# Kernel optimization log

Hardware: AMD Instinct MI355X
Metric: run time of the kernel (lower is better)

The kernel has to match this reference:

```python
import jax, jax.numpy as jnp
import numpy as np

B, C, N, K = 4, 192, 8192, 16
C_OUT = 192


def _gather_nodes(xs, idx):
    # xs: [B, C, N], idx: [B, N, K] -> [B, C, N, K]
    return jax.vmap(lambda xb, ib: xb[:, ib])(xs, idx)


def setup_inputs() -> dict:
    key = jax.random.key(0)
    k1, k2, k3 = jax.random.split(key, 3)
    x = jax.random.normal(k1, (B, C, N, 1), dtype=jnp.float32)
    x_0 = jnp.zeros((B, C, N, 1), dtype=jnp.float32)  # unused by forward, kept for interface
    edge_index = jax.random.randint(k2, (2, B, N, K), 0, N, dtype=jnp.int32)
    # 1x1 Conv2d(2C -> C_OUT) weight flattened to [C_OUT, 2C]
    W = jax.random.normal(k3, (C_OUT, 2 * C), dtype=jnp.float32) / np.sqrt(2 * C)
    b = jnp.zeros((C_OUT,), dtype=jnp.float32)
    return {"x": x, "x_0": x_0, "edge_index": edge_index, "W": W, "b": b}


def reference(x, x_0, edge_index, W, b):
    xs = x[..., 0]                       # [B, C, N]
    x_i = _gather_nodes(xs, edge_index[1])   # centers  [B, C, N, K]
    x_j = _gather_nodes(xs, edge_index[0])   # neighbors [B, C, N, K]
    rel = jnp.max(x_j - x_i, axis=-1)        # max-relative [B, C, N]
    y = jnp.concatenate([xs, rel], axis=1)   # [B, 2C, N]
    out = jnp.einsum('oc,bcn->bon', W, y) + b[None, :, None]  # 1x1 conv
    out = jax.nn.relu(out)
    return out[..., None]                # [B, C_OUT, N, 1]
```

## Files before the change

### kernel.cpp

```cpp
#include <hip/hip_runtime.h>
#include <hip/hip_bf16.h>

#define B_    4
#define C_    192
#define N_    8192
#define K_    16
#define O_    192
#define TWOC_ 384

typedef __attribute__((ext_vector_type(8))) short short8;
typedef __attribute__((ext_vector_type(4))) float floatx4;

static __device__ __forceinline__ float bf2f(unsigned short u) {
    union { unsigned int i; float f; } v; v.i = ((unsigned int)u) << 16; return v.f;
}
static __device__ __forceinline__ unsigned short f2bf(float f) {
    union { float f; unsigned int i; } v; v.f = f;
    unsigned int x = v.i;
    return (unsigned short)((x + 0x7FFFu + ((x >> 16) & 1u)) >> 16);
}

__global__ __launch_bounds__(256) void k_convert_w(const float* __restrict__ W,
                                                   unsigned short* __restrict__ Wb) {
    int i = blockIdx.x * 256 + threadIdx.x;
    if (i < O_ * TWOC_) Wb[i] = f2bf(W[i]);
}

__global__ __launch_bounds__(256) void k_transpose(const float* __restrict__ x,
                                                   unsigned short* __restrict__ yb) {
    __shared__ float tile[32][33];
    int b  = blockIdx.z;
    int c0 = blockIdx.y * 32;
    int n0 = blockIdx.x * 32;
    int tx = threadIdx.x, ty = threadIdx.y;
    const float* xp = x + ((size_t)b * C_ + c0) * N_ + n0;
#pragma unroll
    for (int i = 0; i < 4; i++) {
        int r = ty + 8 * i;
        tile[r][tx] = xp[(size_t)r * N_ + tx];
    }
    __syncthreads();
    unsigned short* yp = yb + ((size_t)b * N_ + n0) * TWOC_ + c0;
#pragma unroll
    for (int i = 0; i < 4; i++) {
        int r = ty + 8 * i;
        yp[(size_t)r * TWOC_ + tx] = f2bf(tile[tx][r]);
    }
}

__global__ __launch_bounds__(256) void k_maxrel(unsigned short* __restrict__ yb,
                                                const int* __restrict__ eidx) {
    int b    = blockIdx.y;
    int wave = threadIdx.x >> 6;
    int lane = threadIdx.x & 63;
    int n    = blockIdx.x * 4 + wave;

    __shared__ int sidx[4][32];
    if (lane < 32) {
        const int* e = eidx + ((size_t)b * N_ + n) * K_;
        int v;
        if (lane < 16) v = e[lane];
        else           v = e[(size_t)B_ * N_ * K_ + (lane - 16)];
        sidx[wave][lane] = v;
    }
    __syncthreads();

    const unsigned short* base = yb + (size_t)b * N_ * TWOC_;
    float m0 = -INFINITY, m1 = -INFINITY, m2 = -INFINITY;
#pragma unroll
    for (int k = 0; k < K_; k++) {
        int j = sidx[wave][k];
        int i = sidx[wave][16 + k];
        const unsigned short* pj = base + (size_t)j * TWOC_;
        const unsigned short* pi = base + (size_t)i * TWOC_;
        float d0 = bf2f(pj[lane])        - bf2f(pi[lane]);
        float d1 = bf2f(pj[lane + 64])   - bf2f(pi[lane + 64]);
        float d2 = bf2f(pj[lane + 128])  - bf2f(pi[lane + 128]);
        m0 = fmaxf(m0, d0);
        m1 = fmaxf(m1, d1);
        m2 = fmaxf(m2, d2);
    }
    unsigned short* w = yb + ((size_t)b * N_ + n) * TWOC_ + C_;
    w[lane]       = f2bf(m0);
    w[lane + 64]  = f2bf(m1);
    w[lane + 128] = f2bf(m2);
}

__global__ __launch_bounds__(64) void k_gemm(const unsigned short* __restrict__ Wb,
                                             const unsigned short* __restrict__ yb,
                                             const float* __restrict__ bias,
                                             float* __restrict__ out) {
    int b    = blockIdx.z;
    int ob   = blockIdx.y;
    int nb   = blockIdx.x;
    int lane = threadIdx.x;
    int m16  = lane & 15;
    int quad = lane >> 4;

    const unsigned short* wbase = Wb + (size_t)(ob * 64 + m16) * TWOC_ + quad * 8;
    const unsigned short* ybase = yb + ((size_t)b * N_ + nb * 64 + m16) * TWOC_ + quad * 8;

    floatx4 acc[4][4];
#pragma unroll
    for (int i = 0; i < 4; i++)
#pragma unroll
        for (int j = 0; j < 4; j++) acc[i][j] = (floatx4){0.f, 0.f, 0.f, 0.f};

#pragma unroll 2
    for (int kt = 0; kt < 12; kt++) {
        short8 af[4], bfr[4];
#pragma unroll
        for (int t = 0; t < 4; t++)
            af[t] = *(const short8*)(wbase + (size_t)(t * 16) * TWOC_ + kt * 32);
#pragma unroll
        for (int t = 0; t < 4; t++)
            bfr[t] = *(const short8*)(ybase + (size_t)(t * 16) * TWOC_ + kt * 32);
#pragma unroll
        for (int i = 0; i < 4; i++)
#pragma unroll
            for (int j = 0; j < 4; j++)
                acc[i][j] = __builtin_amdgcn_mfma_f32_16x16x32_bf16(af[i], bfr[j], acc[i][j], 0, 0, 0);
    }

#pragma unroll
    for (int i = 0; i < 4; i++) {
#pragma unroll
        for (int r = 0; r < 4; r++) {
            int o = ob * 64 + i * 16 + quad * 4 + r;
            float bv = bias[o];
#pragma unroll
            for (int j = 0; j < 4; j++) {
                int n = nb * 64 + j * 16 + m16;
                float v = acc[i][j][r] + bv;
                out[((size_t)b * O_ + o) * N_ + n] = fmaxf(v, 0.f);
            }
        }
    }
}

extern "C" void kernel_launch(void* const* d_in, const int* in_sizes, int n_in,
                              void* d_out, int out_size, void* d_ws, size_t ws_size,
                              hipStream_t stream) {
    const float* x    = (const float*)d_in[0];
    const int*   eidx = (const int*)d_in[2];
    const float* W    = (const float*)d_in[3];
    const float* bias = (const float*)d_in[4];
    float*       out  = (float*)d_out;

    unsigned short* Wb = (unsigned short*)d_ws;
    unsigned short* yb = (unsigned short*)((char*)d_ws + 147456);

    k_convert_w<<<dim3((O_ * TWOC_ + 255) / 256), dim3(256), 0, stream>>>(W, Wb);
    k_transpose<<<dim3(N_ / 32, C_ / 32, B_), dim3(32, 8), 0, stream>>>(x, yb);
    k_maxrel<<<dim3(N_ / 4, B_), dim3(256), 0, stream>>>(yb, eidx);
    k_gemm<<<dim3(N_ / 64, O_ / 64, B_), dim3(64), 0, stream>>>(Wb, yb, bias, out);
}
```

Before: 146.5 us.

## Fuse max-relative gather with GEMM in shared memory, XCD-aware block mapping

Merges the max-relative gather kernel and the 1x1-conv GEMM into one kernel. Each block builds a 64-node tile of [x; rel] in LDS and runs MFMA on it, so the rel half never makes a round trip through global memory. The transpose now writes a compact [B,N,C] bf16 array using vectorized loads and packed stores. Both kernels map blocks so each batch's data stays on a pair of XCDs for L2 locality. The gather loads 4 channels per lane per neighbor. The cost is fewer blocks (512) with a large LDS footprint, which may reduce occupancy and latency hiding for the random gathers.

After: 136.0 us. -7.1%, faster.

```diff
diff --git a/kernel.cpp b/kernel.cpp
--- a/kernel.cpp
+++ b/kernel.cpp
@@ -1,5 +1,4 @@
 #include <hip/hip_runtime.h>
-#include <hip/hip_bf16.h>
 
 #define B_    4
 #define C_    192
@@ -9,10 +8,12 @@
 #define TWOC_ 384
 
 typedef __attribute__((ext_vector_type(8))) short short8;
+typedef __attribute__((ext_vector_type(4))) short short4v;
+typedef __attribute__((ext_vector_type(2))) unsigned int uint2v;
 typedef __attribute__((ext_vector_type(4))) float floatx4;
 
-static __device__ __forceinline__ float bf2f(unsigned short u) {
-    union { unsigned int i; float f; } v; v.i = ((unsigned int)u) << 16; return v.f;
+static __device__ __forceinline__ float bf2f(unsigned int u16) {
+    union { unsigned int i; float f; } v; v.i = u16 << 16; return v.f;
 }
 static __device__ __forceinline__ unsigned short f2bf(float f) {
     union { float f; unsigned int i; } v; v.f = f;
@@ -27,112 +28,155 @@
 }
 
 __global__ __launch_bounds__(256) void k_transpose(const float* __restrict__ x,
-                                                   unsigned short* __restrict__ yb) {
+                                                   unsigned short* __restrict__ xt) {
     __shared__ float tile[32][33];
-    int b  = blockIdx.z;
-    int c0 = blockIdx.y * 32;
-    int n0 = blockIdx.x * 32;
-    int tx = threadIdx.x, ty = threadIdx.y;
-    const float* xp = x + ((size_t)b * C_ + c0) * N_ + n0;
+    int bid  = blockIdx.x;
+    int xcd  = bid & 7;
+    int b    = xcd >> 1;
+    int half = xcd & 1;
+    int slot = bid >> 3;
+    int ct   = slot >> 7;
+    int nt   = half * 128 + (slot & 127);
+    int c0 = ct * 32, n0 = nt * 32;
+    int tid = threadIdx.x;
+
+    int cc  = tid >> 3;
+    int nn4 = (tid & 7) * 4;
+    const float* xp = x + ((size_t)b * C_ + c0 + cc) * N_ + n0 + nn4;
+    float4 v = *(const float4*)xp;
+    tile[nn4 + 0][cc] = v.x;
+    tile[nn4 + 1][cc] = v.y;
+    tile[nn4 + 2][cc] = v.z;
+    tile[nn4 + 3][cc] = v.w;
+    __syncthreads();
+
+#pragma unroll
+    for (int i = 0; i < 2; i++) {
+        int id  = i * 256 + tid;
+        int row = id >> 4;
+        int ch2 = id & 15;
+        float a = tile[row][ch2 * 2];
+        float c = tile[row][ch2 * 2 + 1];
+        unsigned int pack = (unsigned int)f2bf(a) | ((unsigned int)f2bf(c) << 16);
+        *(unsigned int*)(xt + ((size_t)b * N_ + n0 + row) * C_ + c0 + ch2 * 2) = pack;
+    }
+}
+
+__global__ __launch_bounds__(256) void k_fused(const unsigned short* __restrict__ xt,
+                                               const int* __restrict__ eidx,
+                                               const unsigned short* __restrict__ Wb,
+                                               const float* __restrict__ bias,
+                                               float* __restrict__ out) {
+    __shared__ unsigned short ytile[64][TWOC_];
+    __shared__ int sidx[64][33];
+
+    int bid  = blockIdx.x;
+    int xcd  = bid & 7;
+    int b    = xcd >> 1;
+    int slot = bid >> 3;
+    int n0   = ((xcd & 1) * 64 + slot) * 64;
+
+    int tid  = threadIdx.x;
+    int wave = tid >> 6;
+    int lane = tid & 63;
+
+    const int* e0 = eidx + ((size_t)b * N_ + n0) * K_;
+    const int* e1 = e0 + (size_t)B_ * N_ * K_;
 #pragma unroll
     for (int i = 0; i < 4; i++) {
-        int r = ty + 8 * i;
-        tile[r][tx] = xp[(size_t)r * N_ + tx];
+        int id   = i * 256 + tid;
+        int node = id >> 4, k = id & 15;
+        sidx[node][k]      = e0[id];
+        sidx[node][16 + k] = e1[id];
+    }
+
+    const unsigned short* xrow = xt + ((size_t)b * N_ + n0) * C_;
+#pragma unroll
+    for (int i = 0; i < 6; i++) {
+        int id = i * 256 + tid;
+        int row = id / 24, chunk = id % 24;
+        short8 v = *(const short8*)(xrow + (size_t)row * C_ + chunk * 8);
+        *(short8*)&ytile[row][chunk * 8] = v;
     }
     __syncthreads();
-    unsigned short* yp = yb + ((size_t)b * N_ + n0) * TWOC_ + c0;
-#pragma unroll
-    for (int i = 0; i < 4; i++) {
-        int r = ty + 8 * i;
-        yp[(size_t)r * TWOC_ + tx] = f2bf(tile[tx][r]);
-    }
-}
-
-__global__ __launch_bounds__(256) void k_maxrel(unsigned short* __restrict__ yb,
-                                                const int* __restrict__ eidx) {
-    int b    = blockIdx.y;
-    int wave = threadIdx.x >> 6;
-    int lane = threadIdx.x & 63;
-    int n    = blockIdx.x * 4 + wave;
-
-    __shared__ int sidx[4][32];
-    if (lane < 32) {
-        const int* e = eidx + ((size_t)b * N_ + n) * K_;
-        int v;
-        if (lane < 16) v = e[lane];
-        else           v = e[(size_t)B_ * N_ * K_ + (lane - 16)];
-        sidx[wave][lane] = v;
+
+    {
+        int g  = lane >> 4;
+        int l4 = lane & 15;
+        const unsigned short* xbase = xt + (size_t)b * N_ * C_;
+#pragma unroll
+        for (int bb = 0; bb < 4; bb++) {
+            int node = wave * 16 + bb * 4 + g;
+            float m[3][4];
+#pragma unroll
+            for (int t = 0; t < 3; t++)
+#pragma unroll
+                for (int c = 0; c < 4; c++) m[t][c] = -INFINITY;
+#pragma unroll
+            for (int k = 0; k < K_; k++) {
+                int jn = sidx[node][k];
+                int in = sidx[node][16 + k];
+                const unsigned short* pj = xbase + (size_t)jn * C_ + l4 * 4;
+                const unsigned short* pi = xbase + (size_t)in * C_ + l4 * 4;
+#pragma unroll
+                for (int t = 0; t < 3; t++) {
+                    uint2v vj = *(const uint2v*)(pj + t * 64);
+                    uint2v vi = *(const uint2v*)(pi + t * 64);
+                    m[t][0] = fmaxf(m[t][0], bf2f(vj.x & 0xffffu) - bf2f(vi.x & 0xffffu));
+                    m[t][1] = fmaxf(m[t][1], bf2f(vj.x >> 16)     - bf2f(vi.x >> 16));
+                    m[t][2] = fmaxf(m[t][2], bf2f(vj.y & 0xffffu) - bf2f(vi.y & 0xffffu));
+                    m[t][3] = fmaxf(m[t][3], bf2f(vj.y >> 16)     - bf2f(vi.y >> 16));
+                }
+            }
+#pragma unroll
+            for (int t = 0; t < 3; t++) {
+                short4v s;
+                s.x = (short)f2bf(m[t][0]);
+                s.y = (short)f2bf(m[t][1]);
+                s.z = (short)f2bf(m[t][2]);
+                s.w = (short)f2bf(m[t][3]);
+                *(short4v*)&ytile[node][C_ + t * 64 + l4 * 4] = s;
+            }
+        }
     }
     __syncthreads();
 
-    const unsigned short* base = yb + (size_t)b * N_ * TWOC_;
-    float m0 = -INFINITY, m1 = -INFINITY, m2 = -INFINITY;
-#pragma unroll
-    for (int k = 0; k < K_; k++) {
-        int j = sidx[wave][k];
-        int i = sidx[wave][16 + k];
-        const unsigned short* pj = base + (size_t)j * TWOC_;
-        const unsigned short* pi = base + (size_t)i * TWOC_;
-        float d0 = bf2f(pj[lane])        - bf2f(pi[lane]);
-        float d1 = bf2f(pj[lane + 64])   - bf2f(pi[lane + 64]);
-        float d2 = bf2f(pj[lane + 128])  - bf2f(pi[lane + 128]);
-        m0 = fmaxf(m0, d0);
-        m1 = fmaxf(m1, d1);
-        m2 = fmaxf(m2, d2);
-    }
-    unsigned short* w = yb + ((size_t)b * N_ + n) * TWOC_ + C_;
-    w[lane]       = f2bf(m0);
-    w[lane + 64]  = f2bf(m1);
-    w[lane + 128] = f2bf(m2);
-}
-
-__global__ __launch_bounds__(64) void k_gemm(const unsigned short* __restrict__ Wb,
-                                             const unsigned short* __restrict__ yb,
-                                             const float* __restrict__ bias,
-                                             float* __restrict__ out) {
-    int b    = blockIdx.z;
-    int ob   = blockIdx.y;
-    int nb   = blockIdx.x;
-    int lane = threadIdx.x;
     int m16  = lane & 15;
     int quad = lane >> 4;
-
-    const unsigned short* wbase = Wb + (size_t)(ob * 64 + m16) * TWOC_ + quad * 8;
-    const unsigned short* ybase = yb + ((size_t)b * N_ + nb * 64 + m16) * TWOC_ + quad * 8;
-
-    floatx4 acc[4][4];
-#pragma unroll
-    for (int i = 0; i < 4; i++)
+    const unsigned short* wbase = Wb + (size_t)(wave * 48 + m16) * TWOC_ + quad * 8;
+
+    floatx4 acc[3][4];
+#pragma unroll
+    for (int i = 0; i < 3; i++)
 #pragma unroll
         for (int j = 0; j < 4; j++) acc[i][j] = (floatx4){0.f, 0.f, 0.f, 0.f};
 
 #pragma unroll 2
     for (int kt = 0; kt < 12; kt++) {
-        short8 af[4], bfr[4];
-#pragma unroll
-        for (int t = 0; t < 4; t++)
-            af[t] = *(const short8*)(wbase + (size_t)(t * 16) * TWOC_ + kt * 32);
-#pragma unroll
-        for (int t = 0; t < 4; t++)
-            bfr[t] = *(const short8*)(ybase + (size_t)(t * 16) * TWOC_ + kt * 32);
-#pragma unroll
-        for (int i = 0; i < 4; i++)
+        short8 wf[3], yf[4];
+#pragma unroll
+        for (int i = 0; i < 3; i++)
+            wf[i] = *(const short8*)(wbase + (size_t)(i * 16) * TWOC_ + kt * 32);
+#pragma unroll
+        for (int j = 0; j < 4; j++)
+            yf[j] = *(const short8*)&ytile[j * 16 + m16][kt * 32 + quad * 8];
+#pragma unroll
+        for (int i = 0; i < 3; i++)
 #pragma unroll
             for (int j = 0; j < 4; j++)
-                acc[i][j] = __builtin_amdgcn_mfma_f32_16x16x32_bf16(af[i], bfr[j], acc[i][j], 0, 0, 0);
-    }
-
-#pragma unroll
-    for (int i = 0; i < 4; i++) {
+                acc[i][j] = __builtin_amdgcn_mfma_f32_16x16x32_bf16(wf[i], yf[j], acc[i][j], 0, 0, 0);
+    }
+
+#pragma unroll
+    for (int i = 0; i < 3; i++) {
 #pragma unroll
         for (int r = 0; r < 4; r++) {
-            int o = ob * 64 + i * 16 + quad * 4 + r;
+            int o = wave * 48 + i * 16 + quad * 4 + r;
             float bv = bias[o];
 #pragma unroll
             for (int j = 0; j < 4; j++) {
-                int n = nb * 64 + j * 16 + m16;
-                float v = acc[i][j][r] + bv;
-                out[((size_t)b * O_ + o) * N_ + n] = fmaxf(v, 0.f);
+                int n = n0 + j * 16 + m16;
+                out[((size_t)b * O_ + o) * N_ + n] = fmaxf(acc[i][j][r] + bv, 0.f);
             }
         }
     }
@@ -148,10 +192,9 @@
     float*       out  = (float*)d_out;
 
     unsigned short* Wb = (unsigned short*)d_ws;
-    unsigned short* yb = (unsigned short*)((char*)d_ws + 147456);
+    unsigned short* xt = (unsigned short*)((char*)d_ws + 147456);
 
     k_convert_w<<<dim3((O_ * TWOC_ + 255) / 256), dim3(256), 0, stream>>>(W, Wb);
-    k_transpose<<<dim3(N_ / 32, C_ / 32, B_), dim3(32, 8), 0, stream>>>(x, yb);
-    k_maxrel<<<dim3(N_ / 4, B_), dim3(256), 0, stream>>>(yb, eidx);
-    k_gemm<<<dim3(N_ / 64, O_ / 64, B_), dim3(64), 0, stream>>>(Wb, yb, bias, out);
-}
+    k_transpose<<<dim3(6144), dim3(256), 0, stream>>>(x, xt);
+    k_fused<<<dim3(512), dim3(256), 0, stream>>>(xt, eidx, Wb, bias, out);
+}
```
